# Optimization experiments

Hardware: AMD Instinct MI355X
Metric: run time of the kernel (lower is better)

Reference implementation:

```python
import jax, jax.numpy as jnp
import numpy as np


def _bilerp(grid, x, y):
    """Bilinear sample grid [H,W,C] at continuous coords x,y [B,V] -> [B,V,C]."""
    H, W = grid.shape[0], grid.shape[1]
    x0f = jnp.floor(x); y0f = jnp.floor(y)
    wx = (x - x0f)[..., None]; wy = (y - y0f)[..., None]
    x0 = jnp.clip(x0f.astype(jnp.int32), 0, W - 1)
    x1 = jnp.clip(x0f.astype(jnp.int32) + 1, 0, W - 1)
    y0 = jnp.clip(y0f.astype(jnp.int32), 0, H - 1)
    y1 = jnp.clip(y0f.astype(jnp.int32) + 1, 0, H - 1)
    return (grid[y0, x0] * (1 - wx) * (1 - wy) + grid[y0, x1] * wx * (1 - wy)
            + grid[y1, x0] * (1 - wx) * wy + grid[y1, x1] * wx * wy)


def _normalize(x, eps=1e-12):
    n = jnp.linalg.norm(x, axis=-1, keepdims=True)
    return x / jnp.maximum(n, eps)


def setup_inputs() -> dict:
    key = jax.random.key(0)
    ks = jax.random.split(key, 12)
    B, H, W = 4, 512, 512
    V, F = 100000, 200000
    return {
        "vertices": jax.random.normal(ks[0], (1, V, 3), jnp.float32),
        "vertices_texcoords": jax.random.uniform(ks[1], (1, V, 2), jnp.float32),
        "vertices_normals": jax.random.normal(ks[2], (1, V, 3), jnp.float32),
        "faces_vt_idx": jax.random.randint(ks[3], (1, F, 3), 0, V, jnp.int32),
        "faces_vn_idx": jax.random.randint(ks[4], (1, F, 3), 0, V, jnp.int32),
        "faces_v_idx": jax.random.randint(ks[5], (1, F, 3), 0, V, jnp.int32),
        "pose": jax.random.normal(ks[6], (B, 4, 4), jnp.float32),
        "depth": jax.random.uniform(ks[7], (B, H, W), jnp.float32),
        "face_index_map": jax.random.randint(ks[8], (B, H, W), 0, F, jnp.int32),
        "weight_map": jax.random.uniform(ks[9], (B, H, W, 3), jnp.float32),
        "v_uvz": jax.random.uniform(ks[10], (B, V, 3), jnp.float32),
        # +0.5 keeps the z component (used as 1/z) away from zero
        "faces_v_uvz": jax.random.uniform(ks[11], (B, F, 3, 3), jnp.float32) + 0.5,
    }


def reference(vertices, vertices_texcoords, vertices_normals, faces_vt_idx,
              faces_vn_idx, faces_v_idx, pose, depth, face_index_map,
              weight_map, v_uvz, faces_v_uvz):
    B, H, W = depth.shape
    mesh_span = (vertices[0].max(axis=0) - vertices[0].min(axis=0)).max()

    # --- screen-space vertex coords + bilinear depth lookup (front mask) ---
    vx = (v_uvz[..., 0] * 0.5 + 0.5) * W                  # [B,V]
    vy = (1.0 - (v_uvz[..., 1] * 0.5 + 0.5)) * H          # [B,V]
    v_depth = _bilerp(depth[0][..., None], vx, vy)        # [B,V,1] (batch-0 depth, as in source)
    v_front_mask = (v_uvz[0, :, 2] - v_depth[0, :, 0] < mesh_span * 0.005)[None, :]

    # --- perspective-corrected barycentric weights ---
    fz = faces_v_uvz[..., 2]                              # [B,F,3]
    fz_map = jax.vmap(lambda f, idx: f[idx])(fz, face_index_map)  # [B,H,W,3]
    wmap = (1.0 / fz_map) * weight_map * depth[..., None] # [B,H,W,3]
    wmap = wmap[..., None]                                # [B,H,W,3,1]

    # --- uv map ---
    faces_vt = vertices_texcoords[0][faces_vt_idx[0]]     # [F,3,2]
    uv_map = (faces_vt[face_index_map] * wmap).sum(axis=-2)  # [B,H,W,2]
    uv_map = uv_map - jnp.floor(uv_map)

    # --- normal map (object + camera space) ---
    faces_vn = vertices_normals[0][faces_vn_idx[0]]       # [F,3,3]
    normal_map = _normalize((faces_vn[face_index_map] * wmap).sum(axis=-2))
    R = pose[:, :3, :3]
    t = pose[:, :3, -1]
    normal_map_cam = _normalize(jnp.einsum('bij,bhwj->bhwi', R, normal_map))

    # --- position map (object + camera space) ---
    faces_v = vertices[0][faces_v_idx[0]]                 # [F,3,3]
    position_map = (faces_v[face_index_map] * wmap).sum(axis=-2)
    position_map_cam = jnp.einsum('bij,bhwj->bhwi', R, position_map) + t[:, None, None, :]

    # Concatenate float map outputs into one tensor [B,H,W,14]
    out = jnp.concatenate([uv_map, normal_map, normal_map_cam,
                           position_map, position_map_cam], axis=-1)
    return out
```

## Files before the change

kernel.cpp:

```cpp
#include <hip/hip_runtime.h>
#include <stdint.h>


typedef float f4 __attribute__((ext_vector_type(4)));

struct H2 { _Float16 x, y; };
static __device__ __forceinline__ float packh(float a, float b) {
    H2 h; h.x = (_Float16)a; h.y = (_Float16)b;
    return __builtin_bit_cast(float, h);
}
static __device__ __forceinline__ float2 unph(float w) {
    H2 h = __builtin_bit_cast(H2, w);
    return make_float2((float)h.x, (float)h.y);
}

__global__ __launch_bounds__(256) void pack_all(
    const float* __restrict__ tc, const float* __restrict__ nrm,
    const float* __restrict__ vtx,
    const int* __restrict__ f_vt, const int* __restrict__ f_vn,
    const int* __restrict__ f_v,
    const float* __restrict__ fuvz,
    float* __restrict__ rec, float* __restrict__ fzq, int F, int V, int B)
{
    int f = blockIdx.x * 256 + threadIdx.x;
    if (f >= F) return;
    float w[16];
    float h[18];
#pragma unroll
    for (int k = 0; k < 3; ++k) {
        int ivt = f_vt[f * 3 + k];
        ivt = ivt < 0 ? 0 : (ivt >= V ? V - 1 : ivt);
        w[k * 2 + 0] = tc[(long)ivt * 2 + 0];
        w[k * 2 + 1] = tc[(long)ivt * 2 + 1];
        int ivn = f_vn[f * 3 + k];
        ivn = ivn < 0 ? 0 : (ivn >= V ? V - 1 : ivn);
        h[k * 3 + 0] = nrm[(long)ivn * 3 + 0];
        h[k * 3 + 1] = nrm[(long)ivn * 3 + 1];
        h[k * 3 + 2] = nrm[(long)ivn * 3 + 2];
        int iv = f_v[f * 3 + k];
        iv = iv < 0 ? 0 : (iv >= V ? V - 1 : iv);
        h[9 + k * 3 + 0] = vtx[(long)iv * 3 + 0];
        h[9 + k * 3 + 1] = vtx[(long)iv * 3 + 1];
        h[9 + k * 3 + 2] = vtx[(long)iv * 3 + 2];
    }
#pragma unroll
    for (int j = 0; j < 9; ++j)
        w[6 + j] = packh(h[2 * j], h[2 * j + 1]);
    w[15] = 0.0f;
    f4* o = (f4*)(rec + (long)f * 16);
#pragma unroll
    for (int j = 0; j < 4; ++j) {
        f4 t = { w[j * 4], w[j * 4 + 1], w[j * 4 + 2], w[j * 4 + 3] };
        o[j] = t;
    }

    for (int b = 0; b < B; ++b) {
        const float* s = fuvz + ((long)b * F + f) * 9;
        f4 t = { __fdiv_rn(1.0f, s[2]), __fdiv_rn(1.0f, s[5]),
                 __fdiv_rn(1.0f, s[8]), 0.0f };
        ((f4*)fzq)[(long)b * F + f] = t;
    }
}

__global__ __launch_bounds__(256) void raster_fast(
    const float* __restrict__ rec,
    const float* __restrict__ fzq,
    const float* __restrict__ pose,
    const float* __restrict__ depth,
    const int*   __restrict__ fim,
    const float* __restrict__ weight,
    float* __restrict__ out,
    int F, int HW)
{
    __shared__ float sb[256 * 14];
    const int tid = threadIdx.x;
    const int hw  = blockIdx.x * 256 + tid;
    const int b   = blockIdx.y;
    const int p   = b * HW + hw;

    const float* pb = pose + b * 16;
    float R00 = pb[0],  R01 = pb[1],  R02 = pb[2],  t0 = pb[3];
    float R10 = pb[4],  R11 = pb[5],  R12 = pb[6],  t1 = pb[7];
    float R20 = pb[8],  R21 = pb[9],  R22 = pb[10], t2 = pb[11];

    int f = __builtin_nontemporal_load(fim + p);
    f = f < 0 ? 0 : (f >= F ? F - 1 : f);
    const float d = __builtin_nontemporal_load(depth + p);
    float w0 = __builtin_nontemporal_load(weight + (long)p * 3 + 0);
    float w1 = __builtin_nontemporal_load(weight + (long)p * 3 + 1);
    float w2 = __builtin_nontemporal_load(weight + (long)p * 3 + 2);

    const f4* R4 = (const f4*)(rec + (long)f * 16);
    f4 a0 = R4[0], a1 = R4[1], a2 = R4[2], a3 = R4[3];
    f4 fz = ((const f4*)fzq)[(long)b * F + f];

    float wm0 = __fmul_rn(__fmul_rn(fz.x, w0), d);
    float wm1 = __fmul_rn(__fmul_rn(fz.y, w1), d);
    float wm2 = __fmul_rn(__fmul_rn(fz.z, w2), d);

    float uv0 = __fadd_rn(__fadd_rn(__fmul_rn(a0.x, wm0), __fmul_rn(a0.z, wm1)),
                          __fmul_rn(a1.x, wm2));
    float uv1 = __fadd_rn(__fadd_rn(__fmul_rn(a0.y, wm0), __fmul_rn(a0.w, wm1)),
                          __fmul_rn(a1.y, wm2));
    uv0 -= floorf(uv0);
    uv1 -= floorf(uv1);

    float2 g0 = unph(a1.z), g1 = unph(a1.w), g2 = unph(a2.x);
    float2 g3 = unph(a2.y), g4 = unph(a2.z), g5 = unph(a2.w);
    float2 g6 = unph(a3.x), g7 = unph(a3.y), g8 = unph(a3.z);
    float n0 = g0.x * wm0 + g1.y * wm1 + g3.x * wm2;
    float n1 = g0.y * wm0 + g2.x * wm1 + g3.y * wm2;
    float n2 = g1.x * wm0 + g2.y * wm1 + g4.x * wm2;
    float p0 = g4.y * wm0 + g6.x * wm1 + g7.y * wm2;
    float p1 = g5.x * wm0 + g6.y * wm1 + g8.x * wm2;
    float p2 = g5.y * wm0 + g7.x * wm1 + g8.y * wm2;

    float nn = sqrtf(n0 * n0 + n1 * n1 + n2 * n2);
    float ni = 1.0f / fmaxf(nn, 1e-12f);
    float m0 = n0 * ni, m1 = n1 * ni, m2 = n2 * ni;

    float c0 = R00 * m0 + R01 * m1 + R02 * m2;
    float c1 = R10 * m0 + R11 * m1 + R12 * m2;
    float c2 = R20 * m0 + R21 * m1 + R22 * m2;
    float cn = sqrtf(c0 * c0 + c1 * c1 + c2 * c2);
    float ci = 1.0f / fmaxf(cn, 1e-12f);
    c0 *= ci; c1 *= ci; c2 *= ci;

    float q0 = R00 * p0 + R01 * p1 + R02 * p2 + t0;
    float q1 = R10 * p0 + R11 * p1 + R12 * p2 + t1;
    float q2 = R20 * p0 + R21 * p1 + R22 * p2 + t2;

    float* s = sb + tid * 14;
    s[0]  = uv0; s[1]  = uv1;
    s[2]  = m0;  s[3]  = m1;  s[4]  = m2;
    s[5]  = c0;  s[6]  = c1;  s[7]  = c2;
    s[8]  = p0;  s[9]  = p1;  s[10] = p2;
    s[11] = q0;  s[12] = q1;  s[13] = q2;
    __syncthreads();

    f4* og = (f4*)(out + ((long)b * HW + (long)blockIdx.x * 256) * 14);
    const f4* sv = (const f4*)sb;
#pragma unroll
    for (int j = 0; j < 4; ++j) {
        int k = tid + 256 * j;
        if (k < 896) __builtin_nontemporal_store(sv[k], og + k);
    }
}

__global__ __launch_bounds__(256) void raster_kernel(
    const float* __restrict__ vertices, const float* __restrict__ texcoords,
    const float* __restrict__ normals,
    const int* __restrict__ f_vt, const int* __restrict__ f_vn,
    const int* __restrict__ f_v,
    const float* __restrict__ pose, const float* __restrict__ depth,
    const int* __restrict__ fim, const float* __restrict__ weight,
    const float* __restrict__ fuvz, float* __restrict__ out, int F, int V,
    int HW)
{
    const int hw = blockIdx.x * 256 + threadIdx.x;
    if (hw >= HW) return;
    const int b  = blockIdx.y;
    const int p  = b * HW + hw;
    const float* pb = pose + b * 16;
    float R00 = pb[0], R01 = pb[1], R02 = pb[2],  t0 = pb[3];
    float R10 = pb[4], R11 = pb[5], R12 = pb[6],  t1 = pb[7];
    float R20 = pb[8], R21 = pb[9], R22 = pb[10], t2 = pb[11];
    int f = fim[p];
    f = f < 0 ? 0 : (f >= F ? F - 1 : f);
    const float d = depth[p];
    const float* fz = fuvz + ((long)b * F + f) * 9;
    float wm[3];
#pragma unroll
    for (int k = 0; k < 3; ++k)
        wm[k] = __fmul_rn(__fmul_rn(__fdiv_rn(1.0f, fz[k * 3 + 2]),
                                    weight[(long)p * 3 + k]), d);
    float u0t[3], u1t[3];
    float n0 = 0.f, n1 = 0.f, n2 = 0.f, p0 = 0.f, p1 = 0.f, p2 = 0.f;
#pragma unroll
    for (int k = 0; k < 3; ++k) {
        int ivt = f_vt[f * 3 + k], ivn = f_vn[f * 3 + k], iv = f_v[f * 3 + k];
        ivt = ivt < 0 ? 0 : (ivt >= V ? V - 1 : ivt);
        ivn = ivn < 0 ? 0 : (ivn >= V ? V - 1 : ivn);
        iv  = iv  < 0 ? 0 : (iv  >= V ? V - 1 : iv);
        const float* tc = texcoords + (long)ivt * 2;
        u0t[k] = __fmul_rn(tc[0], wm[k]);
        u1t[k] = __fmul_rn(tc[1], wm[k]);
        const float* nr = normals + (long)ivn * 3;
        n0 += nr[0] * wm[k]; n1 += nr[1] * wm[k]; n2 += nr[2] * wm[k];
        const float* vv = vertices + (long)iv * 3;
        p0 += vv[0] * wm[k]; p1 += vv[1] * wm[k]; p2 += vv[2] * wm[k];
    }
    float uv0 = __fadd_rn(__fadd_rn(u0t[0], u0t[1]), u0t[2]);
    float uv1 = __fadd_rn(__fadd_rn(u1t[0], u1t[1]), u1t[2]);
    uv0 -= floorf(uv0); uv1 -= floorf(uv1);
    float nn = sqrtf(n0 * n0 + n1 * n1 + n2 * n2);
    float ni = 1.0f / fmaxf(nn, 1e-12f);
    float m0 = n0 * ni, m1 = n1 * ni, m2 = n2 * ni;
    float c0 = R00 * m0 + R01 * m1 + R02 * m2;
    float c1 = R10 * m0 + R11 * m1 + R12 * m2;
    float c2 = R20 * m0 + R21 * m1 + R22 * m2;
    float cn = sqrtf(c0 * c0 + c1 * c1 + c2 * c2);
    float ci = 1.0f / fmaxf(cn, 1e-12f);
    c0 *= ci; c1 *= ci; c2 *= ci;
    float q0 = R00 * p0 + R01 * p1 + R02 * p2 + t0;
    float q1 = R10 * p0 + R11 * p1 + R12 * p2 + t1;
    float q2 = R20 * p0 + R21 * p1 + R22 * p2 + t2;
    float2* o = (float2*)(out + (long)p * 14);
    o[0] = make_float2(uv0, uv1); o[1] = make_float2(m0, m1);
    o[2] = make_float2(m2, c0);   o[3] = make_float2(c1, c2);
    o[4] = make_float2(p0, p1);   o[5] = make_float2(p2, q0);
    o[6] = make_float2(q1, q2);
}

extern "C" void kernel_launch(void* const* d_in, const int* in_sizes, int n_in,
                              void* d_out, int out_size, void* d_ws, size_t ws_size,
                              hipStream_t stream) {
    const float* vertices  = (const float*)d_in[0];
    const float* texcoords = (const float*)d_in[1];
    const float* normals   = (const float*)d_in[2];
    const int*   f_vt      = (const int*)  d_in[3];
    const int*   f_vn      = (const int*)  d_in[4];
    const int*   f_v       = (const int*)  d_in[5];
    const float* pose      = (const float*)d_in[6];
    const float* depth     = (const float*)d_in[7];
    const int*   fim       = (const int*)  d_in[8];
    const float* weight    = (const float*)d_in[9];
    const float* fuvz      = (const float*)d_in[11];
    float* out = (float*)d_out;

    const int B  = in_sizes[6] / 16;
    const int F  = in_sizes[3] / 3;
    const int V  = in_sizes[1] / 2;
    const int HW = in_sizes[7] / B;

    const size_t rec_bytes = (size_t)F * 64;
    const size_t fzq_bytes = (size_t)B * F * 16;
    const bool ws_ok = d_ws != nullptr &&
                       ws_size >= rec_bytes + fzq_bytes &&
                       (((uintptr_t)d_ws) & 15) == 0 &&
                       (HW % 256) == 0;

    if (ws_ok) {
        float* rec = (float*)d_ws;
        float* fzq = (float*)((char*)d_ws + rec_bytes);
        pack_all<<<(F + 255) / 256, 256, 0, stream>>>(
            texcoords, normals, vertices, f_vt, f_vn, f_v, fuvz,
            rec, fzq, F, V, B);
        dim3 grid(HW / 256, B);
        raster_fast<<<grid, 256, 0, stream>>>(
            rec, fzq, pose, depth, fim, weight, out, F, HW);
    } else {
        dim3 grid((HW + 255) / 256, B);
        raster_kernel<<<grid, 256, 0, stream>>>(
            vertices, texcoords, normals, f_vt, f_vn, f_v,
            pose, depth, fim, weight, fuvz, out, F, V, HW);
    }
}
```

Before: 178.9 us.

## Split face packing into separate kernels and swizzle raster block order

Splits the combined pack kernel into pack_faces, which uses vectorized struct loads for indices and vertex attributes, and a separate pack_fz kernel that gives one thread to each batch-face pair for the reciprocal-z table. This removes the serial per-face loop over the batch. The raster kernel moves to a 1D grid with a swizzle that interleaves the four batches across nearby block IDs, so concurrently running blocks spread across batches. That may change cache and channel behavior for the gathered face records. It costs one extra kernel launch.

```diff
diff --git a/kernel.cpp b/kernel.cpp
--- a/kernel.cpp
+++ b/kernel.cpp
@@ -5,6 +5,8 @@
 typedef float f4 __attribute__((ext_vector_type(4)));
 
 struct H2 { _Float16 x, y; };
+struct F3 { float x, y, z; };
+struct I3 { int x, y, z; };
 static __device__ __forceinline__ float packh(float a, float b) {
     H2 h; h.x = (_Float16)a; h.y = (_Float16)b;
     return __builtin_bit_cast(float, h);
@@ -13,53 +15,55 @@
     H2 h = __builtin_bit_cast(H2, w);
     return make_float2((float)h.x, (float)h.y);
 }
-
-__global__ __launch_bounds__(256) void pack_all(
+static __device__ __forceinline__ int clampi(int v, int hi) {
+    return v < 0 ? 0 : (v >= hi ? hi - 1 : v);
+}
+
+__global__ __launch_bounds__(256) void pack_faces(
     const float* __restrict__ tc, const float* __restrict__ nrm,
     const float* __restrict__ vtx,
     const int* __restrict__ f_vt, const int* __restrict__ f_vn,
     const int* __restrict__ f_v,
-    const float* __restrict__ fuvz,
-    float* __restrict__ rec, float* __restrict__ fzq, int F, int V, int B)
+    float* __restrict__ rec, int F, int V)
 {
     int f = blockIdx.x * 256 + threadIdx.x;
     if (f >= F) return;
+    I3 it = *(const I3*)(f_vt + f * 3);
+    I3 in = *(const I3*)(f_vn + f * 3);
+    I3 iv = *(const I3*)(f_v  + f * 3);
     float w[16];
-    float h[18];
-#pragma unroll
-    for (int k = 0; k < 3; ++k) {
-        int ivt = f_vt[f * 3 + k];
-        ivt = ivt < 0 ? 0 : (ivt >= V ? V - 1 : ivt);
-        w[k * 2 + 0] = tc[(long)ivt * 2 + 0];
-        w[k * 2 + 1] = tc[(long)ivt * 2 + 1];
-        int ivn = f_vn[f * 3 + k];
-        ivn = ivn < 0 ? 0 : (ivn >= V ? V - 1 : ivn);
-        h[k * 3 + 0] = nrm[(long)ivn * 3 + 0];
-        h[k * 3 + 1] = nrm[(long)ivn * 3 + 1];
-        h[k * 3 + 2] = nrm[(long)ivn * 3 + 2];
-        int iv = f_v[f * 3 + k];
-        iv = iv < 0 ? 0 : (iv >= V ? V - 1 : iv);
-        h[9 + k * 3 + 0] = vtx[(long)iv * 3 + 0];
-        h[9 + k * 3 + 1] = vtx[(long)iv * 3 + 1];
-        h[9 + k * 3 + 2] = vtx[(long)iv * 3 + 2];
-    }
-#pragma unroll
-    for (int j = 0; j < 9; ++j)
-        w[6 + j] = packh(h[2 * j], h[2 * j + 1]);
-    w[15] = 0.0f;
+    float2 t0 = *(const float2*)(tc + (long)clampi(it.x, V) * 2);
+    float2 t1 = *(const float2*)(tc + (long)clampi(it.y, V) * 2);
+    float2 t2 = *(const float2*)(tc + (long)clampi(it.z, V) * 2);
+    w[0] = t0.x; w[1] = t0.y; w[2] = t1.x; w[3] = t1.y; w[4] = t2.x; w[5] = t2.y;
+    F3 n0 = *(const F3*)(nrm + (long)clampi(in.x, V) * 3);
+    F3 n1 = *(const F3*)(nrm + (long)clampi(in.y, V) * 3);
+    F3 n2 = *(const F3*)(nrm + (long)clampi(in.z, V) * 3);
+    F3 v0 = *(const F3*)(vtx + (long)clampi(iv.x, V) * 3);
+    F3 v1 = *(const F3*)(vtx + (long)clampi(iv.y, V) * 3);
+    F3 v2 = *(const F3*)(vtx + (long)clampi(iv.z, V) * 3);
+    w[6]  = packh(n0.x, n0.y); w[7]  = packh(n0.z, n1.x);
+    w[8]  = packh(n1.y, n1.z); w[9]  = packh(n2.x, n2.y);
+    w[10] = packh(n2.z, v0.x); w[11] = packh(v0.y, v0.z);
+    w[12] = packh(v1.x, v1.y); w[13] = packh(v1.z, v2.x);
+    w[14] = packh(v2.y, v2.z); w[15] = 0.0f;
     f4* o = (f4*)(rec + (long)f * 16);
 #pragma unroll
     for (int j = 0; j < 4; ++j) {
         f4 t = { w[j * 4], w[j * 4 + 1], w[j * 4 + 2], w[j * 4 + 3] };
         o[j] = t;
     }
-
-    for (int b = 0; b < B; ++b) {
-        const float* s = fuvz + ((long)b * F + f) * 9;
-        f4 t = { __fdiv_rn(1.0f, s[2]), __fdiv_rn(1.0f, s[5]),
-                 __fdiv_rn(1.0f, s[8]), 0.0f };
-        ((f4*)fzq)[(long)b * F + f] = t;
-    }
+}
+
+__global__ __launch_bounds__(256) void pack_fz(
+    const float* __restrict__ fuvz, float* __restrict__ fzq, long BF)
+{
+    long i = (long)blockIdx.x * 256 + threadIdx.x;
+    if (i >= BF) return;
+    const float* s = fuvz + i * 9;
+    f4 t = { __fdiv_rn(1.0f, s[2]), __fdiv_rn(1.0f, s[5]),
+             __fdiv_rn(1.0f, s[8]), 0.0f };
+    ((f4*)fzq)[i] = t;
 }
 
 __global__ __launch_bounds__(256) void raster_fast(
@@ -70,12 +74,20 @@
     const int*   __restrict__ fim,
     const float* __restrict__ weight,
     float* __restrict__ out,
-    int F, int HW)
-{
+    int F, int HW, int nblk, int use_swz)
+{
+    const int id  = blockIdx.x;
+    int b, blk;
+    if (use_swz) {
+        b   = (id & 7) >> 1;
+        blk = ((id >> 3) << 1) | (id & 1);
+    } else {
+        b   = id / nblk;
+        blk = id - b * nblk;
+    }
     __shared__ float sb[256 * 14];
     const int tid = threadIdx.x;
-    const int hw  = blockIdx.x * 256 + tid;
-    const int b   = blockIdx.y;
+    const int hw  = blk * 256 + tid;
     const int p   = b * HW + hw;
 
     const float* pb = pose + b * 16;
@@ -138,7 +150,7 @@
     s[11] = q0;  s[12] = q1;  s[13] = q2;
     __syncthreads();
 
-    f4* og = (f4*)(out + ((long)b * HW + (long)blockIdx.x * 256) * 14);
+    f4* og = (f4*)(out + ((long)b * HW + (long)blk * 256) * 14);
     const f4* sv = (const f4*)sb;
 #pragma unroll
     for (int j = 0; j < 4; ++j) {
@@ -178,10 +190,9 @@
     float n0 = 0.f, n1 = 0.f, n2 = 0.f, p0 = 0.f, p1 = 0.f, p2 = 0.f;
 #pragma unroll
     for (int k = 0; k < 3; ++k) {
-        int ivt = f_vt[f * 3 + k], ivn = f_vn[f * 3 + k], iv = f_v[f * 3 + k];
-        ivt = ivt < 0 ? 0 : (ivt >= V ? V - 1 : ivt);
-        ivn = ivn < 0 ? 0 : (ivn >= V ? V - 1 : ivn);
-        iv  = iv  < 0 ? 0 : (iv  >= V ? V - 1 : iv);
+        int ivt = clampi(f_vt[f * 3 + k], V);
+        int ivn = clampi(f_vn[f * 3 + k], V);
+        int iv  = clampi(f_v [f * 3 + k], V);
         const float* tc = texcoords + (long)ivt * 2;
         u0t[k] = __fmul_rn(tc[0], wm[k]);
         u1t[k] = __fmul_rn(tc[1], wm[k]);
@@ -243,12 +254,14 @@
     if (ws_ok) {
         float* rec = (float*)d_ws;
         float* fzq = (float*)((char*)d_ws + rec_bytes);
-        pack_all<<<(F + 255) / 256, 256, 0, stream>>>(
-            texcoords, normals, vertices, f_vt, f_vn, f_v, fuvz,
-            rec, fzq, F, V, B);
-        dim3 grid(HW / 256, B);
-        raster_fast<<<grid, 256, 0, stream>>>(
-            rec, fzq, pose, depth, fim, weight, out, F, HW);
+        long BF = (long)B * F;
+        pack_faces<<<(F + 255) / 256, 256, 0, stream>>>(
+            texcoords, normals, vertices, f_vt, f_vn, f_v, rec, F, V);
+        pack_fz<<<(unsigned)((BF + 255) / 256), 256, 0, stream>>>(fuvz, fzq, BF);
+        const int nblk = HW / 256;
+        const int use_swz = (B == 4 && (nblk % 2) == 0) ? 1 : 0;
+        raster_fast<<<B * nblk, 256, 0, stream>>>(
+            rec, fzq, pose, depth, fim, weight, out, F, HW, nblk, use_swz);
     } else {
         dim3 grid((HW + 255) / 256, B);
         raster_kernel<<<grid, 256, 0, stream>>>(
```

Result: slower. 184.8 us (+3.3%).
